# Kernel optimization log

Hardware: AMD Instinct MI355X
Metric: run time of the kernel (lower is better)

Reference implementation:

```python
import math
import jax, jax.numpy as jnp
import numpy as np

B, S, H = 4, 2048, 1024

def setup_inputs() -> dict:
    key = jax.random.key(0)
    ks = jax.random.split(key, 7)
    scale = 1.0 / math.sqrt(H)
    return {
        "X":  jax.random.normal(ks[0], (B, S, H), dtype=jnp.float32),
        "Wq": jax.random.normal(ks[1], (H, H), dtype=jnp.float32) * scale,
        "bq": jnp.zeros((H,), dtype=jnp.float32),
        "Wk": jax.random.normal(ks[2], (H, H), dtype=jnp.float32) * scale,
        "bk": jnp.zeros((H,), dtype=jnp.float32),
        "Wv": jax.random.normal(ks[3], (H, H), dtype=jnp.float32) * scale,
        "bv": jnp.zeros((H,), dtype=jnp.float32),
    }

def reference(X, Wq, bq, Wk, bk, Wv, bv):
    # nn.Linear: y = x @ W.T + b
    Q = jnp.einsum("bsh,oh->bso", X, Wq) + bq
    K = jnp.einsum("bsh,oh->bso", X, Wk) + bk
    V = jnp.einsum("bsh,oh->bso", X, Wv) + bv
    hidden_dim = X.shape[-1]
    scores = jnp.einsum("bqh,bkh->bqk", Q, K) / jnp.sqrt(jnp.float32(hidden_dim))
    attn = jax.nn.softmax(scores, axis=-1)  # [B, S, S]
    return jnp.einsum("bqk,bkh->bqh", attn, V)
```

## Files before the change

kernel.cpp:

```cpp
#include <hip/hip_runtime.h>
#include <stdint.h>

#define ASG __attribute__((address_space(1)))
#define ASL __attribute__((address_space(3)))

typedef __bf16 bf16x8 __attribute__((ext_vector_type(8)));
typedef float f32x4 __attribute__((ext_vector_type(4)));

__device__ __forceinline__ unsigned short f2bf(float f) {
  unsigned int u = __builtin_bit_cast(unsigned int, f);
  u = (u + 0x7fffu + ((u >> 16) & 1u)) >> 16;
  return (unsigned short)u;
}

__global__ __launch_bounds__(256) void k_prep(
    const float* __restrict__ X, const float* __restrict__ Wq,
    const float* __restrict__ Wk, const float* __restrict__ Wv,
    const float* __restrict__ bq, const float* __restrict__ bk,
    const float* __restrict__ bv,
    unsigned short* __restrict__ Xb, float* __restrict__ biasF) {
  const int bid = blockIdx.x, tid = threadIdx.x;
  unsigned short* Wb = Xb + 8388608;
  if (bid < 11264) {
    const float* src;
    ushort4* dst;
    int j;
    if (bid < 8192) {
      j = bid * 256 + tid; src = X; dst = (ushort4*)Xb;
    } else {
      int w = (bid - 8192) >> 10;
      j = ((bid - 8192) & 1023) * 256 + tid;
      src = (w == 0) ? Wq : (w == 1 ? Wk : Wv);
      dst = (ushort4*)(Wb + (long)w * 1048576);
    }
    float4 v = reinterpret_cast<const float4*>(src)[j];
    ushort4 o;
    o.x = f2bf(v.x); o.y = f2bf(v.y); o.z = f2bf(v.z); o.w = f2bf(v.w);
    dst[j] = o;
  } else {
    int i = (bid - 11264) * 256 + tid;
    if (i < 3072)
      biasF[i] = (i < 1024) ? bq[i] : (i < 2048 ? bk[i - 1024] : bv[i - 2048]);
  }
}

template <int OUT_MODE, int BIAS>
__global__ __launch_bounds__(512, 4) void gemm3q(
    const unsigned short* __restrict__ A, const unsigned short* __restrict__ B,
    void* __restrict__ Cv, const float* __restrict__ bias,
    int lda, int ldb, int ldc, int K, float alpha,
    long sA, long sB, long sC) {
  __shared__ __align__(16) char smem[73728];
  const int tid = threadIdx.x;
  const int wid = tid >> 6, lane = tid & 63;
  const int wr = wid >> 2, wc = wid & 3;
  const int bm0 = blockIdx.y << 7, bn0 = blockIdx.x << 8;
  A += (long)blockIdx.z * sA;
  B += (long)blockIdx.z * sB;
  const int NT = K >> 5;

  const int srow = tid >> 2;
  const int scol = (((tid & 3) ^ ((srow >> 1) & 3)) << 3);
  long gA0, gB[2];
  gA0 = (long)(bm0 + srow) * lda + scol;
#pragma unroll
  for (int u = 0; u < 2; ++u)
    gB[u] = (long)(bn0 + u * 128 + srow) * ldb + scol;

#define STG(PTR, GOFF, KK, LDSOFF)                                             \
  __builtin_amdgcn_global_load_lds((ASG const void*)((PTR) + (GOFF) + ((KK) << 5)), \
      (ASL void*)(smem + (LDSOFF) + wid * 1024), 16, 0, 0)

#define STG_ALL(KK, SB_) do { int kk = (KK); if (kk >= NT) kk -= NT;           \
    STG(A, gA0, kk, (SB_));                                                    \
    STG(B, gB[0], kk, (SB_) + 8192);                                           \
    STG(B, gB[1], kk, (SB_) + 16384); } while (0)

  const int L = lane & 15;
  const int blk = ((lane >> 4) ^ ((L >> 1) & 3)) << 4;
  int aoff[4], boff[4];
#pragma unroll
  for (int mf = 0; mf < 4; ++mf)
    aoff[mf] = ((wr * 64 + mf * 16 + L) << 6) + blk;
#pragma unroll
  for (int nf = 0; nf < 4; ++nf)
    boff[nf] = 8192 + ((wc * 64 + nf * 16 + L) << 6) + blk;

  bf16x8 afr[4];
  bf16x8 b01[2], b23[2];
  f32x4 acc[4][4] = {};

#define RDA(CB) do { _Pragma("unroll") for (int mf = 0; mf < 4; ++mf)          \
      afr[mf] = *(const bf16x8*)(smem + (CB) + aoff[mf]); } while (0)
#define RDB01(CB) do { _Pragma("unroll") for (int nf = 0; nf < 2; ++nf)        \
      b01[nf] = *(const bf16x8*)(smem + (CB) + boff[nf]); } while (0)
#define RDB23(CB) do { _Pragma("unroll") for (int nf = 0; nf < 2; ++nf)        \
      b23[nf] = *(const bf16x8*)(smem + (CB) + boff[nf + 2]); } while (0)

#define MM(BF, NB) do {                                                        \
    _Pragma("unroll") for (int mf = 0; mf < 4; ++mf)                           \
    _Pragma("unroll") for (int nf = 0; nf < 2; ++nf)                           \
      acc[mf][(NB) + nf] = __builtin_amdgcn_mfma_f32_16x16x32_bf16(            \
          afr[mf], BF[nf], acc[mf][(NB) + nf], 0, 0, 0); } while (0)

  STG_ALL(0, 0);
  STG_ALL(1, 24576);
  asm volatile("s_waitcnt vmcnt(3)" ::: "memory");
  __builtin_amdgcn_s_barrier();
  RDA(0); RDB01(0);

  int bc = 0, bs = 2 * 24576;
  for (int t = 0; t < NT; ++t) {
    RDB23(bc);
    STG_ALL(t + 2, bs);
    __builtin_amdgcn_s_setprio(1);
    MM(b01, 0);
    MM(b23, 2);
    __builtin_amdgcn_s_setprio(0);
    asm volatile("s_waitcnt vmcnt(3) lgkmcnt(0)" ::: "memory");
    __builtin_amdgcn_s_barrier();
    const int bn = (bc == 2 * 24576) ? 0 : bc + 24576;
    if (t + 1 < NT) { RDA(bn); RDB01(bn); }
    bc = bn;
    bs = (bs == 2 * 24576) ? 0 : bs + 24576;
  }

  const int r0 = bm0 + wr * 64 + ((lane >> 4) << 2);
  const int c0 = bn0 + wc * 64 + (lane & 15);
#pragma unroll
  for (int mf = 0; mf < 4; ++mf)
#pragma unroll
    for (int nf = 0; nf < 4; ++nf) {
      const int row0 = r0 + mf * 16;
      const int col = c0 + nf * 16;
      f32x4 v = acc[mf][nf];
      const float bb = BIAS ? bias[col] : 0.0f;
      if (OUT_MODE == 0) {
        unsigned short* C = (unsigned short*)Cv + (long)blockIdx.z * sC;
#pragma unroll
        for (int j = 0; j < 4; ++j)
          C[(long)(row0 + j) * ldc + col] = f2bf(v[j] * alpha + bb);
      } else {
        float* C = (float*)Cv + (long)blockIdx.z * sC;
#pragma unroll
        for (int j = 0; j < 4; ++j)
          C[(long)(row0 + j) * ldc + col] = v[j] * alpha + bb;
      }
    }
#undef STG
#undef STG_ALL
#undef RDA
#undef RDB01
#undef RDB23
#undef MM
}

__global__ __launch_bounds__(256) void k_softmax_bf16(unsigned short* __restrict__ S) {
  long row = blockIdx.x;
  unsigned short* R = S + row * 2048;
  int t = threadIdx.x;
  int wid = t >> 6, lane = t & 63;
  uint4 raw = reinterpret_cast<const uint4*>(R)[t];
  unsigned int w[4] = {raw.x, raw.y, raw.z, raw.w};
  float v[8];
#pragma unroll
  for (int j = 0; j < 4; ++j) {
    v[2 * j]     = __builtin_bit_cast(float, (unsigned int)(w[j] << 16));
    v[2 * j + 1] = __builtin_bit_cast(float, (unsigned int)(w[j] & 0xffff0000u));
  }
  float m = v[0];
#pragma unroll
  for (int j = 1; j < 8; ++j) m = fmaxf(m, v[j]);
#pragma unroll
  for (int off = 32; off >= 1; off >>= 1) m = fmaxf(m, __shfl_xor(m, off));
  __shared__ float red[8];
  if (lane == 0) red[wid] = m;
  __syncthreads();
  m = fmaxf(fmaxf(red[0], red[1]), fmaxf(red[2], red[3]));

  float e[8], s = 0.f;
#pragma unroll
  for (int j = 0; j < 8; ++j) { e[j] = __expf(v[j] - m); s += e[j]; }
#pragma unroll
  for (int off = 32; off >= 1; off >>= 1) s += __shfl_xor(s, off);
  if (lane == 0) red[4 + wid] = s;
  __syncthreads();
  s = red[4] + red[5] + red[6] + red[7];
  float inv = 1.0f / s;

  uint4 o;
  unsigned int* ow = &o.x;
#pragma unroll
  for (int j = 0; j < 4; ++j)
    ow[j] = (unsigned int)f2bf(e[2 * j] * inv) |
            ((unsigned int)f2bf(e[2 * j + 1] * inv) << 16);
  reinterpret_cast<uint4*>(R)[t] = o;
}

__global__ __launch_bounds__(256) void k_transpose_v(const unsigned short* __restrict__ V,
                                                     unsigned short* __restrict__ Vt) {
  __shared__ unsigned short tile[32][33];
  int b = blockIdx.z;
  int s0 = blockIdx.y * 32, h0 = blockIdx.x * 32;
  const unsigned short* Vb = V + (long)b * 2048 * 3072;
  unsigned short* Vtb = Vt + (long)b * 1024 * 2048;
  int tx = threadIdx.x & 31, ty = threadIdx.x >> 5;
#pragma unroll
  for (int i = 0; i < 4; ++i)
    tile[ty + 8 * i][tx] = Vb[(long)(s0 + ty + 8 * i) * 3072 + h0 + tx];
  __syncthreads();
#pragma unroll
  for (int i = 0; i < 4; ++i)
    Vtb[(long)(h0 + ty + 8 * i) * 2048 + s0 + tx] = tile[tx][ty + 8 * i];
}

extern "C" void kernel_launch(void* const* d_in, const int* in_sizes, int n_in,
                              void* d_out, int out_size, void* d_ws, size_t ws_size,
                              hipStream_t stream) {
  const float* X  = (const float*)d_in[0];
  const float* Wq = (const float*)d_in[1];
  const float* bq = (const float*)d_in[2];
  const float* Wk = (const float*)d_in[3];
  const float* bk = (const float*)d_in[4];
  const float* Wv = (const float*)d_in[5];
  const float* bv = (const float*)d_in[6];
  float* out = (float*)d_out;
  (void)in_sizes; (void)n_in; (void)out_size; (void)ws_size;

  constexpr long S = 2048, H = 1024;
  constexpr long MS = 4 * S;

  size_t off = 0;
  auto alloc = [&](size_t bytes) { char* p = (char*)d_ws + off; off += bytes; return p; };
  unsigned short* Xb    = (unsigned short*)alloc(MS * H * 2);
  unsigned short* Wb    = (unsigned short*)alloc(3 * H * H * 2);
  float*          biasF = (float*)alloc(3 * H * 4);
  unsigned short* QKVb  = (unsigned short*)alloc(MS * 3 * H * 2);
  unsigned short* Vt    = (unsigned short*)alloc(4 * H * S * 2);
  unsigned short* Sb    = (unsigned short*)alloc(4 * S * S * 2);
  (void)Wb;

  k_prep<<<dim3(11276), 256, 0, stream>>>(X, Wq, Wk, Wv, bq, bk, bv, Xb, biasF);

  gemm3q<0, 1><<<dim3(12, 64, 1), 512, 0, stream>>>(Xb, Xb + MS * H, QKVb, biasF,
                                                    1024, 1024, 3072, 1024, 1.0f, 0, 0, 0);

  gemm3q<0, 0><<<dim3(8, 16, 4), 512, 0, stream>>>(QKVb, QKVb + 1024, Sb, nullptr,
                                                   3072, 3072, 2048, 1024, 0.03125f,
                                                   S * 3 * H, S * 3 * H, S * S);

  k_softmax_bf16<<<dim3((int)MS), 256, 0, stream>>>(Sb);

  k_transpose_v<<<dim3(32, 64, 4), 256, 0, stream>>>(QKVb + 2048, Vt);

  gemm3q<1, 0><<<dim3(4, 16, 4), 512, 0, stream>>>(Sb, Vt, out, nullptr,
                                                   2048, 2048, 1024, 2048, 1.0f,
                                                   S * S, H * S, S * H);
}
```

Measured before the change: 175.1 us.

## Fuse V transpose into QKV GEMM epilogue and swizzle batched GEMM blocks per XCD

The QKV projection GEMM now writes the V columns directly in transposed layout into Vt, so the separate transpose kernel and its extra read and write of V are removed. The batched QK^T and PV GEMMs use a flattened 1D grid remapped so that each XCD handles a single batch, which is meant to improve L2 reuse of the shared operands. The transposed epilogue writes 8-byte chunks strided by 2048 elements, which is less coalesced than the row-major store, and the plain row-major V is no longer written.

Result: faster. 162.1 us (-7.4%).

```diff
diff --git a/kernel.cpp b/kernel.cpp
--- a/kernel.cpp
+++ b/kernel.cpp
@@ -44,19 +44,31 @@
   }
 }
 
-template <int OUT_MODE, int BIAS>
+template <int OUT_MODE, int BIAS, int SWZ>
 __global__ __launch_bounds__(512, 4) void gemm3q(
     const unsigned short* __restrict__ A, const unsigned short* __restrict__ B,
     void* __restrict__ Cv, const float* __restrict__ bias,
+    unsigned short* __restrict__ VtOut, int nx,
     int lda, int ldb, int ldc, int K, float alpha,
     long sA, long sB, long sC) {
   __shared__ __align__(16) char smem[73728];
   const int tid = threadIdx.x;
   const int wid = tid >> 6, lane = tid & 63;
   const int wr = wid >> 2, wc = wid & 3;
-  const int bm0 = blockIdx.y << 7, bn0 = blockIdx.x << 8;
-  A += (long)blockIdx.z * sA;
-  B += (long)blockIdx.z * sB;
+  int bx, by, bz;
+  if constexpr (SWZ) {
+    const int lid = blockIdx.x;
+    const int xcd = lid & 7;
+    bz = xcd >> 1;
+    const int idx = ((lid >> 3) << 1) + (xcd & 1);
+    bx = idx % nx;
+    by = idx / nx;
+  } else {
+    bx = blockIdx.x; by = blockIdx.y; bz = blockIdx.z;
+  }
+  const int bm0 = by << 7, bn0 = bx << 8;
+  A += (long)bz * sA;
+  B += (long)bz * sB;
   const int NT = K >> 5;
 
   const int srow = tid >> 2;
@@ -127,26 +139,45 @@
 
   const int r0 = bm0 + wr * 64 + ((lane >> 4) << 2);
   const int c0 = bn0 + wc * 64 + (lane & 15);
-#pragma unroll
-  for (int mf = 0; mf < 4; ++mf)
-#pragma unroll
-    for (int nf = 0; nf < 4; ++nf) {
+  if (OUT_MODE == 3 && bn0 >= 2048) {
+#pragma unroll
+    for (int mf = 0; mf < 4; ++mf) {
       const int row0 = r0 + mf * 16;
-      const int col = c0 + nf * 16;
-      f32x4 v = acc[mf][nf];
-      const float bb = BIAS ? bias[col] : 0.0f;
-      if (OUT_MODE == 0) {
-        unsigned short* C = (unsigned short*)Cv + (long)blockIdx.z * sC;
-#pragma unroll
-        for (int j = 0; j < 4; ++j)
-          C[(long)(row0 + j) * ldc + col] = f2bf(v[j] * alpha + bb);
-      } else {
-        float* C = (float*)Cv + (long)blockIdx.z * sC;
-#pragma unroll
-        for (int j = 0; j < 4; ++j)
-          C[(long)(row0 + j) * ldc + col] = v[j] * alpha + bb;
+      const int b = row0 >> 11, s = row0 & 2047;
+      unsigned short* Vb = VtOut + (long)b * 2097152;
+#pragma unroll
+      for (int nf = 0; nf < 4; ++nf) {
+        const int col = c0 + nf * 16;
+        const float bb = BIAS ? bias[col] : 0.0f;
+        f32x4 v = acc[mf][nf];
+        ushort4 o;
+        o.x = f2bf(v[0] * alpha + bb); o.y = f2bf(v[1] * alpha + bb);
+        o.z = f2bf(v[2] * alpha + bb); o.w = f2bf(v[3] * alpha + bb);
+        *reinterpret_cast<ushort4*>(Vb + (long)(col - 2048) * 2048 + s) = o;
       }
     }
+  } else {
+#pragma unroll
+    for (int mf = 0; mf < 4; ++mf)
+#pragma unroll
+      for (int nf = 0; nf < 4; ++nf) {
+        const int row0 = r0 + mf * 16;
+        const int col = c0 + nf * 16;
+        f32x4 v = acc[mf][nf];
+        const float bb = BIAS ? bias[col] : 0.0f;
+        if (OUT_MODE == 0 || OUT_MODE == 3) {
+          unsigned short* C = (unsigned short*)Cv + (long)bz * sC;
+#pragma unroll
+          for (int j = 0; j < 4; ++j)
+            C[(long)(row0 + j) * ldc + col] = f2bf(v[j] * alpha + bb);
+        } else {
+          float* C = (float*)Cv + (long)bz * sC;
+#pragma unroll
+          for (int j = 0; j < 4; ++j)
+            C[(long)(row0 + j) * ldc + col] = v[j] * alpha + bb;
+        }
+      }
+  }
 #undef STG
 #undef STG_ALL
 #undef RDA
@@ -195,23 +226,6 @@
     ow[j] = (unsigned int)f2bf(e[2 * j] * inv) |
             ((unsigned int)f2bf(e[2 * j + 1] * inv) << 16);
   reinterpret_cast<uint4*>(R)[t] = o;
-}
-
-__global__ __launch_bounds__(256) void k_transpose_v(const unsigned short* __restrict__ V,
-                                                     unsigned short* __restrict__ Vt) {
-  __shared__ unsigned short tile[32][33];
-  int b = blockIdx.z;
-  int s0 = blockIdx.y * 32, h0 = blockIdx.x * 32;
-  const unsigned short* Vb = V + (long)b * 2048 * 3072;
-  unsigned short* Vtb = Vt + (long)b * 1024 * 2048;
-  int tx = threadIdx.x & 31, ty = threadIdx.x >> 5;
-#pragma unroll
-  for (int i = 0; i < 4; ++i)
-    tile[ty + 8 * i][tx] = Vb[(long)(s0 + ty + 8 * i) * 3072 + h0 + tx];
-  __syncthreads();
-#pragma unroll
-  for (int i = 0; i < 4; ++i)
-    Vtb[(long)(h0 + ty + 8 * i) * 2048 + s0 + tx] = tile[tx][ty + 8 * i];
 }
 
 extern "C" void kernel_launch(void* const* d_in, const int* in_sizes, int n_in,
@@ -242,18 +256,17 @@
 
   k_prep<<<dim3(11276), 256, 0, stream>>>(X, Wq, Wk, Wv, bq, bk, bv, Xb, biasF);
 
-  gemm3q<0, 1><<<dim3(12, 64, 1), 512, 0, stream>>>(Xb, Xb + MS * H, QKVb, biasF,
-                                                    1024, 1024, 3072, 1024, 1.0f, 0, 0, 0);
-
-  gemm3q<0, 0><<<dim3(8, 16, 4), 512, 0, stream>>>(QKVb, QKVb + 1024, Sb, nullptr,
-                                                   3072, 3072, 2048, 1024, 0.03125f,
-                                                   S * 3 * H, S * 3 * H, S * S);
+  gemm3q<3, 1, 0><<<dim3(12, 64, 1), 512, 0, stream>>>(
+      Xb, Xb + MS * H, QKVb, biasF, Vt, 0,
+      1024, 1024, 3072, 1024, 1.0f, 0, 0, 0);
+
+  gemm3q<0, 0, 1><<<dim3(512), 512, 0, stream>>>(
+      QKVb, QKVb + 1024, Sb, nullptr, nullptr, 8,
+      3072, 3072, 2048, 1024, 0.03125f, S * 3 * H, S * 3 * H, S * S);
 
   k_softmax_bf16<<<dim3((int)MS), 256, 0, stream>>>(Sb);
 
-  k_transpose_v<<<dim3(32, 64, 4), 256, 0, stream>>>(QKVb + 2048, Vt);
-
-  gemm3q<1, 0><<<dim3(4, 16, 4), 512, 0, stream>>>(Sb, Vt, out, nullptr,
-                                                   2048, 2048, 1024, 2048, 1.0f,
-                                                   S * S, H * S, S * H);
-}
+  gemm3q<1, 0, 1><<<dim3(256), 512, 0, stream>>>(
+      Sb, Vt, out, nullptr, nullptr, 4,
+      2048, 2048, 1024, 2048, 1.0f, S * S, H * S, S * H);
+}
```
